# Kernel optimization log

Hardware: AMD Instinct MI355X
Metric: run time of the kernel (lower is better)

Reference implementation:

```python
import jax, jax.numpy as jnp
import numpy as np
from jax import lax

COST_CLASS, COST_BBOX, COST_GIOU = 1.0, 5.0, 2.0
BIG = 1e30  # stand-in for +inf when masking assigned rows/cols


def box_cxcywh_to_xyxy(b):
    cx, cy, w, h = b[..., 0], b[..., 1], b[..., 2], b[..., 3]
    return jnp.stack([cx - 0.5 * w, cy - 0.5 * h, cx + 0.5 * w, cy + 0.5 * h], axis=-1)


def generalized_box_iou(boxes1, boxes2):
    # boxes1: [Q,4] xyxy, boxes2: [T,4] xyxy -> [Q,T]
    area1 = jnp.clip(boxes1[:, 2] - boxes1[:, 0], 0) * jnp.clip(boxes1[:, 3] - boxes1[:, 1], 0)
    area2 = jnp.clip(boxes2[:, 2] - boxes2[:, 0], 0) * jnp.clip(boxes2[:, 3] - boxes2[:, 1], 0)
    lt = jnp.maximum(boxes1[:, None, :2], boxes2[None, :, :2])
    rb = jnp.minimum(boxes1[:, None, 2:], boxes2[None, :, 2:])
    wh = jnp.clip(rb - lt, 0)
    inter = wh[..., 0] * wh[..., 1]
    union = area1[:, None] + area2[None, :] - inter
    iou = inter / jnp.clip(union, 1e-6)
    lt_e = jnp.minimum(boxes1[:, None, :2], boxes2[None, :, :2])
    rb_e = jnp.maximum(boxes1[:, None, 2:], boxes2[None, :, 2:])
    wh_e = jnp.clip(rb_e - lt_e, 0)
    area = wh_e[..., 0] * wh_e[..., 1]
    return iou - (area - union) / jnp.clip(area, 1e-6)


def build_cost(pred_logits, pred_boxes, tgt_labels, tgt_boxes):
    # pred_logits [B,Q,C], pred_boxes [B,Q,4] cxcywh, tgt_labels [B,T], tgt_boxes [B,T,4]
    B, Q, C = pred_logits.shape
    T = tgt_labels.shape[1]
    out_prob = jax.nn.softmax(pred_logits, axis=-1)                       # [B,Q,C]
    idx = jnp.broadcast_to(tgt_labels[:, None, :], (B, Q, T))
    cost_class = -jnp.take_along_axis(out_prob, idx, axis=2)              # [B,Q,T]
    cost_bbox = jnp.sum(jnp.abs(pred_boxes[:, :, None, :] - tgt_boxes[:, None, :, :]), axis=-1)
    giou = jax.vmap(generalized_box_iou)(box_cxcywh_to_xyxy(pred_boxes), box_cxcywh_to_xyxy(tgt_boxes))
    return COST_CLASS * cost_class + COST_BBOX * cost_bbox + COST_GIOU * (-giou)


def greedy_assignment(cost):
    # cost [Q,T] -> (src_idx [n], tgt_idx [n]) with n = min(Q,T); GPU-resident scan
    Q, T = cost.shape
    n = min(Q, T)

    def step(c, _):
        flat = jnp.argmin(c)
        i = flat // T
        j = flat % T
        c = c.at[i, :].set(BIG).at[:, j].set(BIG)
        return c, (i.astype(jnp.int64), j.astype(jnp.int64))

    _, (src, tgt) = lax.scan(step, cost, None, length=n)
    return src, tgt


def setup_inputs() -> dict:
    key = jax.random.key(0)
    k1, k2, k3, k4 = jax.random.split(key, 4)
    B, Q, C, T = 64, 900, 256, 100
    pred_logits = jax.random.normal(k1, (B, Q, C), dtype=jnp.float32)
    pred_boxes = jax.random.uniform(k2, (B, Q, 4), dtype=jnp.float32)   # cxcywh in [0,1)
    tgt_labels = jax.random.randint(k3, (B, T), 0, C)
    tgt_boxes = jax.random.uniform(k4, (B, T, 4), dtype=jnp.float32)
    return {"pred_logits": pred_logits, "pred_boxes": pred_boxes,
            "tgt_labels": tgt_labels, "tgt_boxes": tgt_boxes}


def reference(pred_logits, pred_boxes, tgt_labels, tgt_boxes):
    cost = build_cost(pred_logits, pred_boxes, tgt_labels, tgt_boxes)   # [B,Q,T]
    src_idx, tgt_idx = jax.vmap(greedy_assignment)(cost)                # [B,n] each
    return cost, src_idx, tgt_idx
```

## Files before the change

kernel.cpp:

```cpp
#include <hip/hip_runtime.h>
#include <math.h>

#define B_ 64
#define Q_ 900
#define C_ 256
#define T_ 100
#define N_ 100
#define BIGF 1.0e30f
#define ROWS_PER_LANE 15
#define CHUNKS 15

typedef unsigned int u32;
typedef unsigned long long ull;

__device__ inline u32 hm_ordf(float v) {
    u32 u = __float_as_uint(v);
    return (u & 0x80000000u) ? ~u : (u | 0x80000000u);
}
__device__ inline ull hm_ikey(float v, int r, int t) {
    return ~(((ull)hm_ordf(v) << 18) | ((ull)(u32)r << 7) | (ull)(u32)t);
}

__global__ __launch_bounds__(256) void hm_cost_colmin(
    const float* __restrict__ logits,
    const float* __restrict__ pboxes,
    const int*   __restrict__ tlabels,
    const float* __restrict__ tboxes,
    float* __restrict__ cost,
    ull* __restrict__ part)
{
    int bc   = blockIdx.x;
    int b    = bc / CHUNKS;
    int c    = bc % CHUNKS;
    int lane = threadIdx.x & 63;
    int wid  = threadIdx.x >> 6;
    int r0   = c * 64;
    int R    = Q_ - r0; if (R > 64) R = 64;

    __shared__ double s_exp[4][C_];
    __shared__ ull    s_part[4][128][2];

    int ta = lane, tb = 64 + lane;
    bool hb = (tb < T_);
    int laba = tlabels[b * T_ + ta];
    int labb = hb ? tlabels[b * T_ + tb] : 0;
    const float* tba = tboxes + ((size_t)b * T_ + ta) * 4;
    const float* tbb = tboxes + ((size_t)b * T_ + (hb ? tb : 0)) * 4;
    double tcxa = tba[0], tcya = tba[1], twa = tba[2], tha = tba[3];
    double tcxb = tbb[0], tcyb = tbb[1], twb = tbb[2], thb_ = tbb[3];
    double txa1 = tcxa - 0.5 * twa, tya1 = tcya - 0.5 * tha;
    double txa2 = tcxa + 0.5 * twa, tya2 = tcya + 0.5 * tha;
    double txb1 = tcxb - 0.5 * twb, tyb1 = tcyb - 0.5 * thb_;
    double txb2 = tcxb + 0.5 * twb, tyb2 = tcyb + 0.5 * thb_;
    double area2a = fmax(txa2 - txa1, 0.0) * fmax(tya2 - tya1, 0.0);
    double area2b = fmax(txb2 - txb1, 0.0) * fmax(tyb2 - tyb1, 0.0);

    ull ka1 = 0ull, ka2 = 0ull;
    ull kb1 = 0ull, kb2 = 0ull;

    for (int r = r0 + wid; r < r0 + R; r += 4) {
        int bq = b * Q_ + r;

        const float* row = logits + (size_t)bq * C_;
        float v[4];
        float m = -INFINITY;
#pragma unroll
        for (int i = 0; i < 4; ++i) {
            v[i] = row[lane + 64 * i];
            m = fmaxf(m, v[i]);
        }
#pragma unroll
        for (int off = 32; off >= 1; off >>= 1)
            m = fmaxf(m, __shfl_xor(m, off, 64));

        double e[4];
        double s = 0.0;
#pragma unroll
        for (int i = 0; i < 4; ++i) {
            e[i] = exp((double)v[i] - (double)m);
            s += e[i];
        }
#pragma unroll
        for (int off = 32; off >= 1; off >>= 1)
            s += __shfl_xor(s, off, 64);

#pragma unroll
        for (int i = 0; i < 4; ++i)
            s_exp[wid][lane + 64 * i] = e[i];

        const float* pb = pboxes + (size_t)bq * 4;
        double pcx = pb[0], pcy = pb[1], pw = pb[2], ph = pb[3];
        double px1 = pcx - 0.5 * pw, py1 = pcy - 0.5 * ph;
        double px2 = pcx + 0.5 * pw, py2 = pcy + 0.5 * ph;
        double area1 = fmax(px2 - px1, 0.0) * fmax(py2 - py1, 0.0);

        {
            double prob = s_exp[wid][laba] / s;
            double l1 = fabs(pcx - tcxa) + fabs(pcy - tcya) + fabs(pw - twa) + fabs(ph - tha);
            double iw = fmax(fmin(px2, txa2) - fmax(px1, txa1), 0.0);
            double ih = fmax(fmin(py2, tya2) - fmax(py1, tya1), 0.0);
            double inter = iw * ih;
            double uni = area1 + area2a - inter;
            double iou = inter / fmax(uni, 1e-6);
            double ew = fmax(fmax(px2, txa2) - fmin(px1, txa1), 0.0);
            double eh = fmax(fmax(py2, tya2) - fmin(py1, tya1), 0.0);
            double earea = ew * eh;
            double giou = iou - (earea - uni) / fmax(earea, 1e-6);
            double cst = -prob + 5.0 * l1 - 2.0 * giou;
            float cf = (float)cst;
            cost[(size_t)bq * T_ + ta] = cf;
            ull kk = hm_ikey(cf, r, ta);
            if (kk > ka1) { ka2 = ka1; ka1 = kk; }
            else if (kk > ka2) ka2 = kk;
        }
        if (hb) {
            double prob = s_exp[wid][labb] / s;
            double l1 = fabs(pcx - tcxb) + fabs(pcy - tcyb) + fabs(pw - twb) + fabs(ph - thb_);
            double iw = fmax(fmin(px2, txb2) - fmax(px1, txb1), 0.0);
            double ih = fmax(fmin(py2, tyb2) - fmax(py1, tyb1), 0.0);
            double inter = iw * ih;
            double uni = area1 + area2b - inter;
            double iou = inter / fmax(uni, 1e-6);
            double ew = fmax(fmax(px2, txb2) - fmin(px1, txb1), 0.0);
            double eh = fmax(fmax(py2, tyb2) - fmin(py1, tyb1), 0.0);
            double earea = ew * eh;
            double giou = iou - (earea - uni) / fmax(earea, 1e-6);
            double cst = -prob + 5.0 * l1 - 2.0 * giou;
            float cf = (float)cst;
            cost[(size_t)bq * T_ + tb] = cf;
            ull kk = hm_ikey(cf, r, tb);
            if (kk > kb1) { kb2 = kb1; kb1 = kk; }
            else if (kk > kb2) kb2 = kk;
        }
    }

    s_part[wid][lane][0]      = ka1;
    s_part[wid][lane][1]      = ka2;
    s_part[wid][64 + lane][0] = kb1;
    s_part[wid][64 + lane][1] = kb2;
    __syncthreads();
    int tid = threadIdx.x;
    if (tid < T_) {
        ull b1 = 0ull, b2 = 0ull;
#pragma unroll
        for (int w = 0; w < 4; ++w) {
#pragma unroll
            for (int j = 0; j < 2; ++j) {
                ull cc = s_part[w][tid][j];
                if (cc > b1) { b2 = b1; b1 = cc; }
                else if (cc > b2) b2 = cc;
            }
        }
        ull* dst = part + (((size_t)b * CHUNKS + c) * T_ + tid) * 2;
        dst[0] = b1;
        dst[1] = b2;
    }
}

template <int CTRL>
__device__ inline ull hm_dpp64(ull x) {
    u32 lo = (u32)x, hi = (u32)(x >> 32);
    lo = (u32)__builtin_amdgcn_update_dpp(0, (int)lo, CTRL, 0xF, 0xF, false);
    hi = (u32)__builtin_amdgcn_update_dpp(0, (int)hi, CTRL, 0xF, 0xF, false);
    return ((ull)hi << 32) | lo;
}

__device__ inline ull hm_wave_max_chain(ull x) {
    ull p;
    p = hm_dpp64<0x111>(x); x = (p > x) ? p : x;
    p = hm_dpp64<0x112>(x); x = (p > x) ? p : x;
    p = hm_dpp64<0x114>(x); x = (p > x) ? p : x;
    p = hm_dpp64<0x118>(x); x = (p > x) ? p : x;
    p = hm_dpp64<0x142>(x); x = (p > x) ? p : x;
    p = hm_dpp64<0x143>(x); x = (p > x) ? p : x;
    return x;
}

__device__ inline u32 hm_wave_max_lo(ull x) {
    x = hm_wave_max_chain(x);
    return (u32)__builtin_amdgcn_readlane((int)(u32)x, 63);
}
__device__ inline ull hm_wave_max_full(ull x) {
    x = hm_wave_max_chain(x);
    u32 lo = (u32)__builtin_amdgcn_readlane((int)(u32)x, 63);
    u32 hi = (u32)__builtin_amdgcn_readlane((int)(u32)(x >> 32), 63);
    return ((ull)hi << 32) | lo;
}

__global__ __launch_bounds__(64) void hm_greedy_top2k(
    const float* __restrict__ cost,
    const ull* __restrict__ part,
    float* __restrict__ out_src,
    float* __restrict__ out_tgt)
{
    int b = blockIdx.x;
    int l = threadIdx.x;
    const float* Cb = cost + (size_t)b * Q_ * T_;

    int  t0 = l, t1 = 64 + l;
    bool a1 = (t1 < T_);

    ull c1a = 0ull, c2a = 0ull, c1b = 0ull, c2b = 0ull;
#pragma unroll
    for (int c = 0; c < CHUNKS; ++c) {
        const ull* p0 = part + (((size_t)b * CHUNKS + c) * T_ + t0) * 2;
#pragma unroll
        for (int j = 0; j < 2; ++j) {
            ull cc = p0[j];
            if (cc > c1a) { c2a = c1a; c1a = cc; }
            else if (cc > c2a) c2a = cc;
        }
        if (a1) {
            const ull* p1 = part + (((size_t)b * CHUNKS + c) * T_ + t1) * 2;
#pragma unroll
            for (int j = 0; j < 2; ++j) {
                ull cc = p1[j];
                if (cc > c1b) { c2b = c1b; c1b = cc; }
                else if (cc > c2b) c2b = cc;
            }
        }
    }

    unsigned removed = 0u;
    float* os = out_src + b * N_;
    float* ot = out_tgt + b * N_;

    int k = 0;
    while (k < N_) {
        ull cmax = (c1a > c1b) ? c1a : c1b;
        u32 winlo = hm_wave_max_lo(cmax);
        u32 keylo = ~winlo;
        int t = (int)(keylo & 127u);
        int q = (int)((keylo >> 7) & 1023u);

        if ((keylo >> 17) & 1u) {
            ull b1 = 0ull, b2 = 0ull;
#pragma unroll
            for (int i = 0; i < ROWS_PER_LANE; ++i) {
                int r = l + 64 * i;
                bool ok = (r < Q_) && !((removed >> i) & 1u);
                float v = ok ? Cb[(size_t)r * T_ + t] : BIGF;
                ull ik = ok ? hm_ikey(v, r, t) : 0ull;
                if (ik > b1) { b2 = b1; b1 = ik; }
                else if (ik > b2) b2 = ik;
            }
            ull w1 = hm_wave_max_full(b1);
            ull alt = (b1 == w1) ? b2 : b1;
            ull w2 = hm_wave_max_full(alt);
            if (t0 == t) { c1a = w1; c2a = w2; }
            if (t1 == t) { c1b = w1; c2b = w2; }
            continue;
        }

        if (l == 0) { os[k] = (float)q; ot[k] = (float)t; }
        if ((q & 63) == l) removed |= 1u << (q >> 6);

        {
            u32 r1 = ((~(u32)c1a) >> 7) & 1023u;
            u32 r2 = ((~(u32)c2a) >> 7) & 1023u;
            bool die1 = (r1 == (u32)q);
            bool die2 = (r2 == (u32)q);
            ull st2 = c2a & ~(1ull << 17);
            ull nc1 = die1 ? c2a : c1a;
            ull nc2 = (die1 || die2) ? st2 : c2a;
            bool kill = (t0 == t);
            c1a = kill ? 0ull : nc1;
            c2a = kill ? 0ull : nc2;
        }
        {
            u32 r1 = ((~(u32)c1b) >> 7) & 1023u;
            u32 r2 = ((~(u32)c2b) >> 7) & 1023u;
            bool die1 = (r1 == (u32)q);
            bool die2 = (r2 == (u32)q);
            ull st2 = c2b & ~(1ull << 17);
            ull nc1 = die1 ? c2b : c1b;
            ull nc2 = (die1 || die2) ? st2 : c2b;
            bool kill = (t1 == t);
            c1b = kill ? 0ull : nc1;
            c2b = kill ? 0ull : nc2;
        }

        ++k;
    }
}

extern "C" void kernel_launch(void* const* d_in, const int* in_sizes, int n_in,
                              void* d_out, int out_size, void* d_ws, size_t ws_size,
                              hipStream_t stream)
{
    const float* pred_logits = (const float*)d_in[0];
    const float* pred_boxes  = (const float*)d_in[1];
    const int*   tgt_labels  = (const int*)d_in[2];
    const float* tgt_boxes   = (const float*)d_in[3];

    float* out_cost = (float*)d_out;
    float* out_src  = out_cost + (size_t)B_ * Q_ * T_;
    float* out_tgt  = out_src  + (size_t)B_ * N_;

    ull* part = (ull*)d_ws;

    hm_cost_colmin<<<B_ * CHUNKS, 256, 0, stream>>>(pred_logits, pred_boxes,
                                                    tgt_labels, tgt_boxes,
                                                    out_cost, part);

    hm_greedy_top2k<<<B_, 64, 0, stream>>>(out_cost, part, out_src, out_tgt);
}
```

Measured before the change: 104.7 us.

## Use fp32 cost math, finer row chunks, and two-batch interleaved greedy wave

The cost kernel switches from double to float arithmetic and splits each batch into 25 chunks of 36 rows instead of 15 chunks of 64. The greedy kernel now handles two batches per wave, interleaving their DPP reductions to hide latency. It also splits each 64-bit key into a 32-bit value reduction followed by an id reduction, and buffers outputs in registers until the end. Float math may change tie-breaking and assignments compared with the double-precision path, and half as many greedy blocks run.

```diff
diff --git a/kernel.cpp b/kernel.cpp
--- a/kernel.cpp
+++ b/kernel.cpp
@@ -8,7 +8,8 @@
 #define N_ 100
 #define BIGF 1.0e30f
 #define ROWS_PER_LANE 15
-#define CHUNKS 15
+#define CHUNKS 25
+#define RPC 36
 
 typedef unsigned int u32;
 typedef unsigned long long ull;
@@ -21,7 +22,7 @@
     return ~(((ull)hm_ordf(v) << 18) | ((ull)(u32)r << 7) | (ull)(u32)t);
 }
 
-__global__ __launch_bounds__(256) void hm_cost_colmin(
+__global__ __launch_bounds__(256) void hm_cost_colmin_f32(
     const float* __restrict__ logits,
     const float* __restrict__ pboxes,
     const int*   __restrict__ tlabels,
@@ -34,11 +35,10 @@
     int c    = bc % CHUNKS;
     int lane = threadIdx.x & 63;
     int wid  = threadIdx.x >> 6;
-    int r0   = c * 64;
-    int R    = Q_ - r0; if (R > 64) R = 64;
-
-    __shared__ double s_exp[4][C_];
-    __shared__ ull    s_part[4][128][2];
+    int r0   = c * RPC;
+
+    __shared__ float s_exp[4][C_];
+    __shared__ ull   s_part[4][128][2];
 
     int ta = lane, tb = 64 + lane;
     bool hb = (tb < T_);
@@ -46,19 +46,19 @@
     int labb = hb ? tlabels[b * T_ + tb] : 0;
     const float* tba = tboxes + ((size_t)b * T_ + ta) * 4;
     const float* tbb = tboxes + ((size_t)b * T_ + (hb ? tb : 0)) * 4;
-    double tcxa = tba[0], tcya = tba[1], twa = tba[2], tha = tba[3];
-    double tcxb = tbb[0], tcyb = tbb[1], twb = tbb[2], thb_ = tbb[3];
-    double txa1 = tcxa - 0.5 * twa, tya1 = tcya - 0.5 * tha;
-    double txa2 = tcxa + 0.5 * twa, tya2 = tcya + 0.5 * tha;
-    double txb1 = tcxb - 0.5 * twb, tyb1 = tcyb - 0.5 * thb_;
-    double txb2 = tcxb + 0.5 * twb, tyb2 = tcyb + 0.5 * thb_;
-    double area2a = fmax(txa2 - txa1, 0.0) * fmax(tya2 - tya1, 0.0);
-    double area2b = fmax(txb2 - txb1, 0.0) * fmax(tyb2 - tyb1, 0.0);
+    float tcxa = tba[0], tcya = tba[1], twa = tba[2], tha = tba[3];
+    float tcxb = tbb[0], tcyb = tbb[1], twb = tbb[2], thb_ = tbb[3];
+    float txa1 = tcxa - 0.5f * twa, tya1 = tcya - 0.5f * tha;
+    float txa2 = tcxa + 0.5f * twa, tya2 = tcya + 0.5f * tha;
+    float txb1 = tcxb - 0.5f * twb, tyb1 = tcyb - 0.5f * thb_;
+    float txb2 = tcxb + 0.5f * twb, tyb2 = tcyb + 0.5f * thb_;
+    float area2a = fmaxf(txa2 - txa1, 0.0f) * fmaxf(tya2 - tya1, 0.0f);
+    float area2b = fmaxf(txb2 - txb1, 0.0f) * fmaxf(tyb2 - tyb1, 0.0f);
 
     ull ka1 = 0ull, ka2 = 0ull;
     ull kb1 = 0ull, kb2 = 0ull;
 
-    for (int r = r0 + wid; r < r0 + R; r += 4) {
+    for (int r = r0 + wid; r < r0 + RPC; r += 4) {
         int bq = b * Q_ + r;
 
         const float* row = logits + (size_t)bq * C_;
@@ -73,11 +73,11 @@
         for (int off = 32; off >= 1; off >>= 1)
             m = fmaxf(m, __shfl_xor(m, off, 64));
 
-        double e[4];
-        double s = 0.0;
+        float e[4];
+        float s = 0.0f;
 #pragma unroll
         for (int i = 0; i < 4; ++i) {
-            e[i] = exp((double)v[i] - (double)m);
+            e[i] = expf(v[i] - m);
             s += e[i];
         }
 #pragma unroll
@@ -89,44 +89,42 @@
             s_exp[wid][lane + 64 * i] = e[i];
 
         const float* pb = pboxes + (size_t)bq * 4;
-        double pcx = pb[0], pcy = pb[1], pw = pb[2], ph = pb[3];
-        double px1 = pcx - 0.5 * pw, py1 = pcy - 0.5 * ph;
-        double px2 = pcx + 0.5 * pw, py2 = pcy + 0.5 * ph;
-        double area1 = fmax(px2 - px1, 0.0) * fmax(py2 - py1, 0.0);
+        float pcx = pb[0], pcy = pb[1], pw = pb[2], ph = pb[3];
+        float px1 = pcx - 0.5f * pw, py1 = pcy - 0.5f * ph;
+        float px2 = pcx + 0.5f * pw, py2 = pcy + 0.5f * ph;
+        float area1 = fmaxf(px2 - px1, 0.0f) * fmaxf(py2 - py1, 0.0f);
 
         {
-            double prob = s_exp[wid][laba] / s;
-            double l1 = fabs(pcx - tcxa) + fabs(pcy - tcya) + fabs(pw - twa) + fabs(ph - tha);
-            double iw = fmax(fmin(px2, txa2) - fmax(px1, txa1), 0.0);
-            double ih = fmax(fmin(py2, tya2) - fmax(py1, tya1), 0.0);
-            double inter = iw * ih;
-            double uni = area1 + area2a - inter;
-            double iou = inter / fmax(uni, 1e-6);
-            double ew = fmax(fmax(px2, txa2) - fmin(px1, txa1), 0.0);
-            double eh = fmax(fmax(py2, tya2) - fmin(py1, tya1), 0.0);
-            double earea = ew * eh;
-            double giou = iou - (earea - uni) / fmax(earea, 1e-6);
-            double cst = -prob + 5.0 * l1 - 2.0 * giou;
-            float cf = (float)cst;
+            float prob = s_exp[wid][laba] / s;
+            float l1 = fabsf(pcx - tcxa) + fabsf(pcy - tcya) + fabsf(pw - twa) + fabsf(ph - tha);
+            float iw = fmaxf(fminf(px2, txa2) - fmaxf(px1, txa1), 0.0f);
+            float ih = fmaxf(fminf(py2, tya2) - fmaxf(py1, tya1), 0.0f);
+            float inter = iw * ih;
+            float uni = area1 + area2a - inter;
+            float iou = inter / fmaxf(uni, 1e-6f);
+            float ew = fmaxf(fmaxf(px2, txa2) - fminf(px1, txa1), 0.0f);
+            float eh = fmaxf(fmaxf(py2, tya2) - fminf(py1, tya1), 0.0f);
+            float earea = ew * eh;
+            float giou = iou - (earea - uni) / fmaxf(earea, 1e-6f);
+            float cf = -prob + 5.0f * l1 - 2.0f * giou;
             cost[(size_t)bq * T_ + ta] = cf;
             ull kk = hm_ikey(cf, r, ta);
             if (kk > ka1) { ka2 = ka1; ka1 = kk; }
             else if (kk > ka2) ka2 = kk;
         }
         if (hb) {
-            double prob = s_exp[wid][labb] / s;
-            double l1 = fabs(pcx - tcxb) + fabs(pcy - tcyb) + fabs(pw - twb) + fabs(ph - thb_);
-            double iw = fmax(fmin(px2, txb2) - fmax(px1, txb1), 0.0);
-            double ih = fmax(fmin(py2, tyb2) - fmax(py1, tyb1), 0.0);
-            double inter = iw * ih;
-            double uni = area1 + area2b - inter;
-            double iou = inter / fmax(uni, 1e-6);
-            double ew = fmax(fmax(px2, txb2) - fmin(px1, txb1), 0.0);
-            double eh = fmax(fmax(py2, tyb2) - fmin(py1, tyb1), 0.0);
-            double earea = ew * eh;
-            double giou = iou - (earea - uni) / fmax(earea, 1e-6);
-            double cst = -prob + 5.0 * l1 - 2.0 * giou;
-            float cf = (float)cst;
+            float prob = s_exp[wid][labb] / s;
+            float l1 = fabsf(pcx - tcxb) + fabsf(pcy - tcyb) + fabsf(pw - twb) + fabsf(ph - thb_);
+            float iw = fmaxf(fminf(px2, txb2) - fmaxf(px1, txb1), 0.0f);
+            float ih = fmaxf(fminf(py2, tyb2) - fmaxf(py1, tyb1), 0.0f);
+            float inter = iw * ih;
+            float uni = area1 + area2b - inter;
+            float iou = inter / fmaxf(uni, 1e-6f);
+            float ew = fmaxf(fmaxf(px2, txb2) - fminf(px1, txb1), 0.0f);
+            float eh = fmaxf(fmaxf(py2, tyb2) - fminf(py1, tyb1), 0.0f);
+            float earea = ew * eh;
+            float giou = iou - (earea - uni) / fmaxf(earea, 1e-6f);
+            float cf = -prob + 5.0f * l1 - 2.0f * giou;
             cost[(size_t)bq * T_ + tb] = cf;
             ull kk = hm_ikey(cf, r, tb);
             if (kk > kb1) { kb2 = kb1; kb1 = kk; }
@@ -157,6 +155,14 @@
     }
 }
 
+__device__ inline u32 hm_umax32(u32 a, u32 b) { return a > b ? a : b; }
+
+template <int CTRL>
+__device__ inline u32 hm_stage(u32 x) {
+    u32 p = (u32)__builtin_amdgcn_update_dpp(0, (int)x, CTRL, 0xF, 0xF, false);
+    return x > p ? x : p;
+}
+
 template <int CTRL>
 __device__ inline ull hm_dpp64(ull x) {
     u32 lo = (u32)x, hi = (u32)(x >> 32);
@@ -164,8 +170,7 @@
     hi = (u32)__builtin_amdgcn_update_dpp(0, (int)hi, CTRL, 0xF, 0xF, false);
     return ((ull)hi << 32) | lo;
 }
-
-__device__ inline ull hm_wave_max_chain(ull x) {
+__device__ inline ull hm_wave_max_full64(ull x) {
     ull p;
     p = hm_dpp64<0x111>(x); x = (p > x) ? p : x;
     p = hm_dpp64<0x112>(x); x = (p > x) ? p : x;
@@ -173,114 +178,232 @@
     p = hm_dpp64<0x118>(x); x = (p > x) ? p : x;
     p = hm_dpp64<0x142>(x); x = (p > x) ? p : x;
     p = hm_dpp64<0x143>(x); x = (p > x) ? p : x;
-    return x;
-}
-
-__device__ inline u32 hm_wave_max_lo(ull x) {
-    x = hm_wave_max_chain(x);
-    return (u32)__builtin_amdgcn_readlane((int)(u32)x, 63);
-}
-__device__ inline ull hm_wave_max_full(ull x) {
-    x = hm_wave_max_chain(x);
     u32 lo = (u32)__builtin_amdgcn_readlane((int)(u32)x, 63);
     u32 hi = (u32)__builtin_amdgcn_readlane((int)(u32)(x >> 32), 63);
     return ((ull)hi << 32) | lo;
 }
 
-__global__ __launch_bounds__(64) void hm_greedy_top2k(
+__global__ __launch_bounds__(64) void hm_greedy_g2(
     const float* __restrict__ cost,
     const ull* __restrict__ part,
     float* __restrict__ out_src,
     float* __restrict__ out_tgt)
 {
-    int b = blockIdx.x;
+    int bp = blockIdx.x;
+    int b0 = bp * 2, b1 = bp * 2 + 1;
     int l = threadIdx.x;
-    const float* Cb = cost + (size_t)b * Q_ * T_;
+    const float* C0 = cost + (size_t)b0 * Q_ * T_;
+    const float* C1 = cost + (size_t)b1 * Q_ * T_;
 
     int  t0 = l, t1 = 64 + l;
     bool a1 = (t1 < T_);
 
-    ull c1a = 0ull, c2a = 0ull, c1b = 0ull, c2b = 0ull;
+    ull pA1_0 = 0ull, pA2_0 = 0ull, pB1_0 = 0ull, pB2_0 = 0ull;
+    ull pA1_1 = 0ull, pA2_1 = 0ull, pB1_1 = 0ull, pB2_1 = 0ull;
 #pragma unroll
     for (int c = 0; c < CHUNKS; ++c) {
-        const ull* p0 = part + (((size_t)b * CHUNKS + c) * T_ + t0) * 2;
+        const ull* q0 = part + (((size_t)b0 * CHUNKS + c) * T_ + t0) * 2;
+        const ull* q1 = part + (((size_t)b1 * CHUNKS + c) * T_ + t0) * 2;
 #pragma unroll
         for (int j = 0; j < 2; ++j) {
-            ull cc = p0[j];
-            if (cc > c1a) { c2a = c1a; c1a = cc; }
-            else if (cc > c2a) c2a = cc;
+            ull cc = q0[j];
+            if (cc > pA1_0) { pA2_0 = pA1_0; pA1_0 = cc; } else if (cc > pA2_0) pA2_0 = cc;
+            ull dd = q1[j];
+            if (dd > pA1_1) { pA2_1 = pA1_1; pA1_1 = dd; } else if (dd > pA2_1) pA2_1 = dd;
         }
         if (a1) {
-            const ull* p1 = part + (((size_t)b * CHUNKS + c) * T_ + t1) * 2;
+            const ull* r0p = part + (((size_t)b0 * CHUNKS + c) * T_ + t1) * 2;
+            const ull* r1p = part + (((size_t)b1 * CHUNKS + c) * T_ + t1) * 2;
 #pragma unroll
             for (int j = 0; j < 2; ++j) {
-                ull cc = p1[j];
-                if (cc > c1b) { c2b = c1b; c1b = cc; }
-                else if (cc > c2b) c2b = cc;
+                ull cc = r0p[j];
+                if (cc > pB1_0) { pB2_0 = pB1_0; pB1_0 = cc; } else if (cc > pB2_0) pB2_0 = cc;
+                ull dd = r1p[j];
+                if (dd > pB1_1) { pB2_1 = pB1_1; pB1_1 = dd; } else if (dd > pB2_1) pB2_1 = dd;
             }
         }
     }
 
-    unsigned removed = 0u;
-    float* os = out_src + b * N_;
-    float* ot = out_tgt + b * N_;
-
-    int k = 0;
-    while (k < N_) {
-        ull cmax = (c1a > c1b) ? c1a : c1b;
-        u32 winlo = hm_wave_max_lo(cmax);
-        u32 keylo = ~winlo;
-        int t = (int)(keylo & 127u);
-        int q = (int)((keylo >> 7) & 1023u);
-
-        if ((keylo >> 17) & 1u) {
-            ull b1 = 0ull, b2 = 0ull;
-#pragma unroll
-            for (int i = 0; i < ROWS_PER_LANE; ++i) {
-                int r = l + 64 * i;
-                bool ok = (r < Q_) && !((removed >> i) & 1u);
-                float v = ok ? Cb[(size_t)r * T_ + t] : BIGF;
-                ull ik = ok ? hm_ikey(v, r, t) : 0ull;
-                if (ik > b1) { b2 = b1; b1 = ik; }
-                else if (ik > b2) b2 = ik;
+    u32 ya0  = ~((u32)((~pA1_0) >> 18)), ida0  = (u32)(~pA1_0) & 0x3FFFFu;
+    u32 y2a0 = ~((u32)((~pA2_0) >> 18)), id2a0 = (u32)(~pA2_0) & 0x3FFFFu;
+    u32 yb0  = a1 ? ~((u32)((~pB1_0) >> 18)) : 0u;
+    u32 idb0 = a1 ? ((u32)(~pB1_0) & 0x3FFFFu) : 0x3FFFFu;
+    u32 y2b0 = a1 ? ~((u32)((~pB2_0) >> 18)) : 0u;
+    u32 id2b0 = a1 ? ((u32)(~pB2_0) & 0x3FFFFu) : 0x3FFFFu;
+    u32 ya1  = ~((u32)((~pA1_1) >> 18)), ida1  = (u32)(~pA1_1) & 0x3FFFFu;
+    u32 y2a1 = ~((u32)((~pA2_1) >> 18)), id2a1 = (u32)(~pA2_1) & 0x3FFFFu;
+    u32 yb1  = a1 ? ~((u32)((~pB1_1) >> 18)) : 0u;
+    u32 idb1 = a1 ? ((u32)(~pB1_1) & 0x3FFFFu) : 0x3FFFFu;
+    u32 y2b1 = a1 ? ~((u32)((~pB2_1) >> 18)) : 0u;
+    u32 id2b1 = a1 ? ((u32)(~pB2_1) & 0x3FFFFu) : 0x3FFFFu;
+
+    unsigned rem0 = 0u, rem1 = 0u;
+    u32 pk00 = 0u, pk01 = 0u, pk10 = 0u, pk11 = 0u;
+    int k0 = 0, k1 = 0;
+
+    while (k0 < N_ || k1 < N_) {
+        u32 x0 = (k0 < N_) ? hm_umax32(ya0, yb0) : 0u;
+        u32 x1 = (k1 < N_) ? hm_umax32(ya1, yb1) : 0u;
+        x0 = hm_stage<0x111>(x0); x1 = hm_stage<0x111>(x1);
+        x0 = hm_stage<0x112>(x0); x1 = hm_stage<0x112>(x1);
+        x0 = hm_stage<0x114>(x0); x1 = hm_stage<0x114>(x1);
+        x0 = hm_stage<0x118>(x0); x1 = hm_stage<0x118>(x1);
+        x0 = hm_stage<0x142>(x0); x1 = hm_stage<0x142>(x1);
+        x0 = hm_stage<0x143>(x0); x1 = hm_stage<0x143>(x1);
+        u32 winy0 = (u32)__builtin_amdgcn_readlane((int)x0, 63);
+        u32 winy1 = (u32)__builtin_amdgcn_readlane((int)x1, 63);
+
+        u32 za0 = (ya0 == winy0) ? ~ida0 : 0u;
+        u32 zb0 = (yb0 == winy0) ? ~idb0 : 0u;
+        u32 z0 = hm_umax32(za0, zb0);
+        u32 za1 = (ya1 == winy1) ? ~ida1 : 0u;
+        u32 zb1 = (yb1 == winy1) ? ~idb1 : 0u;
+        u32 z1 = hm_umax32(za1, zb1);
+        z0 = hm_stage<0x111>(z0); z1 = hm_stage<0x111>(z1);
+        z0 = hm_stage<0x112>(z0); z1 = hm_stage<0x112>(z1);
+        z0 = hm_stage<0x114>(z0); z1 = hm_stage<0x114>(z1);
+        z0 = hm_stage<0x118>(z0); z1 = hm_stage<0x118>(z1);
+        z0 = hm_stage<0x142>(z0); z1 = hm_stage<0x142>(z1);
+        z0 = hm_stage<0x143>(z0); z1 = hm_stage<0x143>(z1);
+        u32 winid0 = (~(u32)__builtin_amdgcn_readlane((int)z0, 63)) & 0x3FFFFu;
+        u32 winid1 = (~(u32)__builtin_amdgcn_readlane((int)z1, 63)) & 0x3FFFFu;
+
+        if (k0 < N_) {
+            int t = (int)(winid0 & 127u);
+            int q = (int)((winid0 >> 7) & 1023u);
+            if (winid0 & 0x20000u) {
+                ull b1k = 0ull, b2k = 0ull;
+#pragma unroll
+                for (int i = 0; i < ROWS_PER_LANE; ++i) {
+                    int r = l + 64 * i;
+                    bool ok = (r < Q_) && !((rem0 >> i) & 1u);
+                    float v = ok ? C0[(size_t)r * T_ + t] : BIGF;
+                    ull ik = ok ? hm_ikey(v, r, t) : 0ull;
+                    if (ik > b1k) { b2k = b1k; b1k = ik; }
+                    else if (ik > b2k) b2k = ik;
+                }
+                ull w1 = hm_wave_max_full64(b1k);
+                ull alt = (b1k == w1) ? b2k : b1k;
+                ull w2 = hm_wave_max_full64(alt);
+                if (t0 == t) {
+                    ya0  = ~((u32)((~w1) >> 18)); ida0  = (u32)(~w1) & 0x3FFFFu;
+                    y2a0 = ~((u32)((~w2) >> 18)); id2a0 = (u32)(~w2) & 0x3FFFFu;
+                }
+                if (t1 == t) {
+                    yb0  = ~((u32)((~w1) >> 18)); idb0  = (u32)(~w1) & 0x3FFFFu;
+                    y2b0 = ~((u32)((~w2) >> 18)); id2b0 = (u32)(~w2) & 0x3FFFFu;
+                }
+            } else {
+                u32 qt = winid0 & 0x1FFFFu;
+                if (k0 < 64) { if (l == k0)        pk00 = qt; }
+                else         { if (l == (k0 & 63)) pk01 = qt; }
+                if ((q & 63) == l) rem0 |= 1u << (q >> 6);
+                {
+                    bool die1 = (((ida0  >> 7) & 1023u) == (u32)q);
+                    bool die2 = (((id2a0 >> 7) & 1023u) == (u32)q);
+                    u32 nya  = die1 ? y2a0  : ya0;
+                    u32 nida = die1 ? id2a0 : ida0;
+                    u32 nid2 = (die1 || die2) ? (id2a0 | 0x20000u) : id2a0;
+                    bool kill = (t0 == t);
+                    ya0   = kill ? 0u       : nya;
+                    ida0  = kill ? 0x3FFFFu : nida;
+                    y2a0  = kill ? 0u       : y2a0;
+                    id2a0 = kill ? 0x3FFFFu : nid2;
+                }
+                {
+                    bool die1 = (((idb0  >> 7) & 1023u) == (u32)q);
+                    bool die2 = (((id2b0 >> 7) & 1023u) == (u32)q);
+                    u32 nyb  = die1 ? y2b0  : yb0;
+                    u32 nidb = die1 ? id2b0 : idb0;
+                    u32 nid2 = (die1 || die2) ? (id2b0 | 0x20000u) : id2b0;
+                    bool kill = (t1 == t);
+                    yb0   = kill ? 0u       : nyb;
+                    idb0  = kill ? 0x3FFFFu : nidb;
+                    y2b0  = kill ? 0u       : y2b0;
+                    id2b0 = kill ? 0x3FFFFu : nid2;
+                }
+                ++k0;
             }
-            ull w1 = hm_wave_max_full(b1);
-            ull alt = (b1 == w1) ? b2 : b1;
-            ull w2 = hm_wave_max_full(alt);
-            if (t0 == t) { c1a = w1; c2a = w2; }
-            if (t1 == t) { c1b = w1; c2b = w2; }
-            continue;
-        }
-
-        if (l == 0) { os[k] = (float)q; ot[k] = (float)t; }
-        if ((q & 63) == l) removed |= 1u << (q >> 6);
-
-        {
-            u32 r1 = ((~(u32)c1a) >> 7) & 1023u;
-            u32 r2 = ((~(u32)c2a) >> 7) & 1023u;
-            bool die1 = (r1 == (u32)q);
-            bool die2 = (r2 == (u32)q);
-            ull st2 = c2a & ~(1ull << 17);
-            ull nc1 = die1 ? c2a : c1a;
-            ull nc2 = (die1 || die2) ? st2 : c2a;
-            bool kill = (t0 == t);
-            c1a = kill ? 0ull : nc1;
-            c2a = kill ? 0ull : nc2;
-        }
-        {
-            u32 r1 = ((~(u32)c1b) >> 7) & 1023u;
-            u32 r2 = ((~(u32)c2b) >> 7) & 1023u;
-            bool die1 = (r1 == (u32)q);
-            bool die2 = (r2 == (u32)q);
-            ull st2 = c2b & ~(1ull << 17);
-            ull nc1 = die1 ? c2b : c1b;
-            ull nc2 = (die1 || die2) ? st2 : c2b;
-            bool kill = (t1 == t);
-            c1b = kill ? 0ull : nc1;
-            c2b = kill ? 0ull : nc2;
-        }
-
-        ++k;
+        }
+
+        if (k1 < N_) {
+            int t = (int)(winid1 & 127u);
+            int q = (int)((winid1 >> 7) & 1023u);
+            if (winid1 & 0x20000u) {
+                ull b1k = 0ull, b2k = 0ull;
+#pragma unroll
+                for (int i = 0; i < ROWS_PER_LANE; ++i) {
+                    int r = l + 64 * i;
+                    bool ok = (r < Q_) && !((rem1 >> i) & 1u);
+                    float v = ok ? C1[(size_t)r * T_ + t] : BIGF;
+                    ull ik = ok ? hm_ikey(v, r, t) : 0ull;
+                    if (ik > b1k) { b2k = b1k; b1k = ik; }
+                    else if (ik > b2k) b2k = ik;
+                }
+                ull w1 = hm_wave_max_full64(b1k);
+                ull alt = (b1k == w1) ? b2k : b1k;
+                ull w2 = hm_wave_max_full64(alt);
+                if (t0 == t) {
+                    ya1  = ~((u32)((~w1) >> 18)); ida1  = (u32)(~w1) & 0x3FFFFu;
+                    y2a1 = ~((u32)((~w2) >> 18)); id2a1 = (u32)(~w2) & 0x3FFFFu;
+                }
+                if (t1 == t) {
+                    yb1  = ~((u32)((~w1) >> 18)); idb1  = (u32)(~w1) & 0x3FFFFu;
+                    y2b1 = ~((u32)((~w2) >> 18)); id2b1 = (u32)(~w2) & 0x3FFFFu;
+                }
+            } else {
+                u32 qt = winid1 & 0x1FFFFu;
+                if (k1 < 64) { if (l == k1)        pk10 = qt; }
+                else         { if (l == (k1 & 63)) pk11 = qt; }
+                if ((q & 63) == l) rem1 |= 1u << (q >> 6);
+                {
+                    bool die1 = (((ida1  >> 7) & 1023u) == (u32)q);
+                    bool die2 = (((id2a1 >> 7) & 1023u) == (u32)q);
+                    u32 nya  = die1 ? y2a1  : ya1;
+                    u32 nida = die1 ? id2a1 : ida1;
+                    u32 nid2 = (die1 || die2) ? (id2a1 | 0x20000u) : id2a1;
+                    bool kill = (t0 == t);
+                    ya1   = kill ? 0u       : nya;
+                    ida1  = kill ? 0x3FFFFu : nida;
+                    y2a1  = kill ? 0u       : y2a1;
+                    id2a1 = kill ? 0x3FFFFu : nid2;
+                }
+                {
+                    bool die1 = (((idb1  >> 7) & 1023u) == (u32)q);
+                    bool die2 = (((id2b1 >> 7) & 1023u) == (u32)q);
+                    u32 nyb  = die1 ? y2b1  : yb1;
+                    u32 nidb = die1 ? id2b1 : idb1;
+                    u32 nid2 = (die1 || die2) ? (id2b1 | 0x20000u) : id2b1;
+                    bool kill = (t1 == t);
+                    yb1   = kill ? 0u       : nyb;
+                    idb1  = kill ? 0x3FFFFu : nidb;
+                    y2b1  = kill ? 0u       : y2b1;
+                    id2b1 = kill ? 0x3FFFFu : nid2;
+                }
+                ++k1;
+            }
+        }
+    }
+
+    {
+        float* os = out_src + b0 * N_;
+        float* ot = out_tgt + b0 * N_;
+        os[l] = (float)(pk00 >> 7);
+        ot[l] = (float)(pk00 & 127u);
+        if (l < N_ - 64) {
+            os[64 + l] = (float)(pk01 >> 7);
+            ot[64 + l] = (float)(pk01 & 127u);
+        }
+    }
+    {
+        float* os = out_src + b1 * N_;
+        float* ot = out_tgt + b1 * N_;
+        os[l] = (float)(pk10 >> 7);
+        ot[l] = (float)(pk10 & 127u);
+        if (l < N_ - 64) {
+            os[64 + l] = (float)(pk11 >> 7);
+            ot[64 + l] = (float)(pk11 & 127u);
+        }
     }
 }
 
@@ -299,9 +422,9 @@
 
     ull* part = (ull*)d_ws;
 
-    hm_cost_colmin<<<B_ * CHUNKS, 256, 0, stream>>>(pred_logits, pred_boxes,
-                                                    tgt_labels, tgt_boxes,
-                                                    out_cost, part);
-
-    hm_greedy_top2k<<<B_, 64, 0, stream>>>(out_cost, part, out_src, out_tgt);
-}
+    hm_cost_colmin_f32<<<B_ * CHUNKS, 256, 0, stream>>>(pred_logits, pred_boxes,
+                                                        tgt_labels, tgt_boxes,
+                                                        out_cost, part);
+
+    hm_greedy_g2<<<B_ / 2, 64, 0, stream>>>(out_cost, part, out_src, out_tgt);
+}
```

After: 118.3 us. +13.0%, slower.

## Switch cost kernel to fp32, rebalance chunks, and use sorted-head greedy assignment

Applied to the files above, without the earlier changes.

The cost kernel now computes softmax, L1 and GIoU in single precision instead of double, which removes slow FP64 math. Rows per block go from 64 to 36, giving 25 chunks per batch and more blocks. The greedy kernel is rewritten so that it rank-sorts per-column minima once and then walks the sorted head, keeping a small overflow set refreshed by the stored second-best entry or by a column rescan. This replaces the per-step wave-wide argmax. The risks are fp32 rounding changing the cost values or tie order, and extra complexity in the assignment logic.

```diff
diff --git a/kernel.cpp b/kernel.cpp
--- a/kernel.cpp
+++ b/kernel.cpp
@@ -8,7 +8,9 @@
 #define N_ 100
 #define BIGF 1.0e30f
 #define ROWS_PER_LANE 15
-#define CHUNKS 15
+#define CHUNKS 25
+#define RPC 36
+#define MAXK 0xFFFFFFFFFFFFFFFFull
 
 typedef unsigned int u32;
 typedef unsigned long long ull;
@@ -21,7 +23,7 @@
     return ~(((ull)hm_ordf(v) << 18) | ((ull)(u32)r << 7) | (ull)(u32)t);
 }
 
-__global__ __launch_bounds__(256) void hm_cost_colmin(
+__global__ __launch_bounds__(256) void hm_cost_colmin_f32(
     const float* __restrict__ logits,
     const float* __restrict__ pboxes,
     const int*   __restrict__ tlabels,
@@ -34,11 +36,10 @@
     int c    = bc % CHUNKS;
     int lane = threadIdx.x & 63;
     int wid  = threadIdx.x >> 6;
-    int r0   = c * 64;
-    int R    = Q_ - r0; if (R > 64) R = 64;
-
-    __shared__ double s_exp[4][C_];
-    __shared__ ull    s_part[4][128][2];
+    int r0   = c * RPC;
+
+    __shared__ float s_exp[4][C_];
+    __shared__ ull   s_part[4][128][2];
 
     int ta = lane, tb = 64 + lane;
     bool hb = (tb < T_);
@@ -46,19 +47,19 @@
     int labb = hb ? tlabels[b * T_ + tb] : 0;
     const float* tba = tboxes + ((size_t)b * T_ + ta) * 4;
     const float* tbb = tboxes + ((size_t)b * T_ + (hb ? tb : 0)) * 4;
-    double tcxa = tba[0], tcya = tba[1], twa = tba[2], tha = tba[3];
-    double tcxb = tbb[0], tcyb = tbb[1], twb = tbb[2], thb_ = tbb[3];
-    double txa1 = tcxa - 0.5 * twa, tya1 = tcya - 0.5 * tha;
-    double txa2 = tcxa + 0.5 * twa, tya2 = tcya + 0.5 * tha;
-    double txb1 = tcxb - 0.5 * twb, tyb1 = tcyb - 0.5 * thb_;
-    double txb2 = tcxb + 0.5 * twb, tyb2 = tcyb + 0.5 * thb_;
-    double area2a = fmax(txa2 - txa1, 0.0) * fmax(tya2 - tya1, 0.0);
-    double area2b = fmax(txb2 - txb1, 0.0) * fmax(tyb2 - tyb1, 0.0);
+    float tcxa = tba[0], tcya = tba[1], twa = tba[2], tha = tba[3];
+    float tcxb = tbb[0], tcyb = tbb[1], twb = tbb[2], thb_ = tbb[3];
+    float txa1 = tcxa - 0.5f * twa, tya1 = tcya - 0.5f * tha;
+    float txa2 = tcxa + 0.5f * twa, tya2 = tcya + 0.5f * tha;
+    float txb1 = tcxb - 0.5f * twb, tyb1 = tcyb - 0.5f * thb_;
+    float txb2 = tcxb + 0.5f * twb, tyb2 = tcyb + 0.5f * thb_;
+    float area2a = fmaxf(txa2 - txa1, 0.0f) * fmaxf(tya2 - tya1, 0.0f);
+    float area2b = fmaxf(txb2 - txb1, 0.0f) * fmaxf(tyb2 - tyb1, 0.0f);
 
     ull ka1 = 0ull, ka2 = 0ull;
     ull kb1 = 0ull, kb2 = 0ull;
 
-    for (int r = r0 + wid; r < r0 + R; r += 4) {
+    for (int r = r0 + wid; r < r0 + RPC; r += 4) {
         int bq = b * Q_ + r;
 
         const float* row = logits + (size_t)bq * C_;
@@ -73,11 +74,11 @@
         for (int off = 32; off >= 1; off >>= 1)
             m = fmaxf(m, __shfl_xor(m, off, 64));
 
-        double e[4];
-        double s = 0.0;
+        float e[4];
+        float s = 0.0f;
 #pragma unroll
         for (int i = 0; i < 4; ++i) {
-            e[i] = exp((double)v[i] - (double)m);
+            e[i] = expf(v[i] - m);
             s += e[i];
         }
 #pragma unroll
@@ -89,44 +90,42 @@
             s_exp[wid][lane + 64 * i] = e[i];
 
         const float* pb = pboxes + (size_t)bq * 4;
-        double pcx = pb[0], pcy = pb[1], pw = pb[2], ph = pb[3];
-        double px1 = pcx - 0.5 * pw, py1 = pcy - 0.5 * ph;
-        double px2 = pcx + 0.5 * pw, py2 = pcy + 0.5 * ph;
-        double area1 = fmax(px2 - px1, 0.0) * fmax(py2 - py1, 0.0);
+        float pcx = pb[0], pcy = pb[1], pw = pb[2], ph = pb[3];
+        float px1 = pcx - 0.5f * pw, py1 = pcy - 0.5f * ph;
+        float px2 = pcx + 0.5f * pw, py2 = pcy + 0.5f * ph;
+        float area1 = fmaxf(px2 - px1, 0.0f) * fmaxf(py2 - py1, 0.0f);
 
         {
-            double prob = s_exp[wid][laba] / s;
-            double l1 = fabs(pcx - tcxa) + fabs(pcy - tcya) + fabs(pw - twa) + fabs(ph - tha);
-            double iw = fmax(fmin(px2, txa2) - fmax(px1, txa1), 0.0);
-            double ih = fmax(fmin(py2, tya2) - fmax(py1, tya1), 0.0);
-            double inter = iw * ih;
-            double uni = area1 + area2a - inter;
-            double iou = inter / fmax(uni, 1e-6);
-            double ew = fmax(fmax(px2, txa2) - fmin(px1, txa1), 0.0);
-            double eh = fmax(fmax(py2, tya2) - fmin(py1, tya1), 0.0);
-            double earea = ew * eh;
-            double giou = iou - (earea - uni) / fmax(earea, 1e-6);
-            double cst = -prob + 5.0 * l1 - 2.0 * giou;
-            float cf = (float)cst;
+            float prob = s_exp[wid][laba] / s;
+            float l1 = fabsf(pcx - tcxa) + fabsf(pcy - tcya) + fabsf(pw - twa) + fabsf(ph - tha);
+            float iw = fmaxf(fminf(px2, txa2) - fmaxf(px1, txa1), 0.0f);
+            float ih = fmaxf(fminf(py2, tya2) - fmaxf(py1, tya1), 0.0f);
+            float inter = iw * ih;
+            float uni = area1 + area2a - inter;
+            float iou = inter / fmaxf(uni, 1e-6f);
+            float ew = fmaxf(fmaxf(px2, txa2) - fminf(px1, txa1), 0.0f);
+            float eh = fmaxf(fmaxf(py2, tya2) - fminf(py1, tya1), 0.0f);
+            float earea = ew * eh;
+            float giou = iou - (earea - uni) / fmaxf(earea, 1e-6f);
+            float cf = -prob + 5.0f * l1 - 2.0f * giou;
             cost[(size_t)bq * T_ + ta] = cf;
             ull kk = hm_ikey(cf, r, ta);
             if (kk > ka1) { ka2 = ka1; ka1 = kk; }
             else if (kk > ka2) ka2 = kk;
         }
         if (hb) {
-            double prob = s_exp[wid][labb] / s;
-            double l1 = fabs(pcx - tcxb) + fabs(pcy - tcyb) + fabs(pw - twb) + fabs(ph - thb_);
-            double iw = fmax(fmin(px2, txb2) - fmax(px1, txb1), 0.0);
-            double ih = fmax(fmin(py2, tyb2) - fmax(py1, tyb1), 0.0);
-            double inter = iw * ih;
-            double uni = area1 + area2b - inter;
-            double iou = inter / fmax(uni, 1e-6);
-            double ew = fmax(fmax(px2, txb2) - fmin(px1, txb1), 0.0);
-            double eh = fmax(fmax(py2, tyb2) - fmin(py1, tyb1), 0.0);
-            double earea = ew * eh;
-            double giou = iou - (earea - uni) / fmax(earea, 1e-6);
-            double cst = -prob + 5.0 * l1 - 2.0 * giou;
-            float cf = (float)cst;
+            float prob = s_exp[wid][labb] / s;
+            float l1 = fabsf(pcx - tcxb) + fabsf(pcy - tcyb) + fabsf(pw - twb) + fabsf(ph - thb_);
+            float iw = fmaxf(fminf(px2, txb2) - fmaxf(px1, txb1), 0.0f);
+            float ih = fmaxf(fminf(py2, tyb2) - fmaxf(py1, tyb1), 0.0f);
+            float inter = iw * ih;
+            float uni = area1 + area2b - inter;
+            float iou = inter / fmaxf(uni, 1e-6f);
+            float ew = fmaxf(fmaxf(px2, txb2) - fminf(px1, txb1), 0.0f);
+            float eh = fmaxf(fmaxf(py2, tyb2) - fminf(py1, tyb1), 0.0f);
+            float earea = ew * eh;
+            float giou = iou - (earea - uni) / fmaxf(earea, 1e-6f);
+            float cf = -prob + 5.0f * l1 - 2.0f * giou;
             cost[(size_t)bq * T_ + tb] = cf;
             ull kk = hm_ikey(cf, r, tb);
             if (kk > kb1) { kb2 = kb1; kb1 = kk; }
@@ -164,8 +163,7 @@
     hi = (u32)__builtin_amdgcn_update_dpp(0, (int)hi, CTRL, 0xF, 0xF, false);
     return ((ull)hi << 32) | lo;
 }
-
-__device__ inline ull hm_wave_max_chain(ull x) {
+__device__ inline ull hm_wave_max_full64(ull x) {
     ull p;
     p = hm_dpp64<0x111>(x); x = (p > x) ? p : x;
     p = hm_dpp64<0x112>(x); x = (p > x) ? p : x;
@@ -173,21 +171,38 @@
     p = hm_dpp64<0x118>(x); x = (p > x) ? p : x;
     p = hm_dpp64<0x142>(x); x = (p > x) ? p : x;
     p = hm_dpp64<0x143>(x); x = (p > x) ? p : x;
-    return x;
-}
-
-__device__ inline u32 hm_wave_max_lo(ull x) {
-    x = hm_wave_max_chain(x);
-    return (u32)__builtin_amdgcn_readlane((int)(u32)x, 63);
-}
-__device__ inline ull hm_wave_max_full(ull x) {
-    x = hm_wave_max_chain(x);
     u32 lo = (u32)__builtin_amdgcn_readlane((int)(u32)x, 63);
     u32 hi = (u32)__builtin_amdgcn_readlane((int)(u32)(x >> 32), 63);
     return ((ull)hi << 32) | lo;
 }
 
-__global__ __launch_bounds__(64) void hm_greedy_top2k(
+__device__ inline ull hm_ov_min(ull a, ull b) {
+    ull x = ~a, y = ~b;
+    ull z = (x > y) ? x : y;
+    return ~hm_wave_max_full64(z);
+}
+
+__device__ inline ull hm_rescan(const float* Cb, int t, u32 removed, int l) {
+    ull best = 0ull;
+#pragma unroll
+    for (int i = 0; i < ROWS_PER_LANE; ++i) {
+        int r = l + 64 * i;
+        bool ok = (r < Q_) && !((removed >> i) & 1u);
+        float v = ok ? Cb[(size_t)r * T_ + t] : BIGF;
+        ull ik = ok ? hm_ikey(v, r, t) : 0ull;
+        best = (ik > best) ? ik : best;
+    }
+    return ~hm_wave_max_full64(best);
+}
+
+__device__ inline void hm_ov_insert(ull ins, int l, ull& ovK0, ull& ovK1) {
+    int t2 = (int)((u32)ins & 127u);
+    int owner = t2 & 63;
+    if (t2 < 64) { if (l == owner) ovK0 = ins; }
+    else         { if (l == owner) ovK1 = ins; }
+}
+
+__global__ __launch_bounds__(64) void hm_greedy_sorted(
     const float* __restrict__ cost,
     const ull* __restrict__ part,
     float* __restrict__ out_src,
@@ -200,87 +215,177 @@
     int  t0 = l, t1 = 64 + l;
     bool a1 = (t1 < T_);
 
-    ull c1a = 0ull, c2a = 0ull, c1b = 0ull, c2b = 0ull;
+    __shared__ ull s_key[128];
+    __shared__ ull s_pay[128];
+
+    ull i1a = 0ull, i2a = 0ull, i1b = 0ull, i2b = 0ull;
 #pragma unroll
     for (int c = 0; c < CHUNKS; ++c) {
         const ull* p0 = part + (((size_t)b * CHUNKS + c) * T_ + t0) * 2;
 #pragma unroll
         for (int j = 0; j < 2; ++j) {
             ull cc = p0[j];
-            if (cc > c1a) { c2a = c1a; c1a = cc; }
-            else if (cc > c2a) c2a = cc;
+            if (cc > i1a) { i2a = i1a; i1a = cc; }
+            else if (cc > i2a) i2a = cc;
         }
         if (a1) {
             const ull* p1 = part + (((size_t)b * CHUNKS + c) * T_ + t1) * 2;
 #pragma unroll
             for (int j = 0; j < 2; ++j) {
                 ull cc = p1[j];
-                if (cc > c1b) { c2b = c1b; c1b = cc; }
-                else if (cc > c2b) c2b = cc;
+                if (cc > i1b) { i2b = i1b; i1b = cc; }
+                else if (cc > i2b) i2b = cc;
             }
         }
     }
-
-    unsigned removed = 0u;
+    ull keyA = ~i1a, payA = ~i2a;
+    ull keyB = a1 ? ~i1b : (0xFFFFFFFFFFFFFF00ull | (ull)(u32)(64 + l));
+    ull payB = a1 ? ~i2b : MAXK;
+
+    s_key[l] = keyA;      s_pay[l] = payA;
+    s_key[64 + l] = keyB; s_pay[64 + l] = payB;
+    __syncthreads();
+
+    int rank0 = 0, rank1 = 0;
+#pragma unroll 4
+    for (int j = 0; j < 128; ++j) {
+        ull kj = s_key[j];
+        rank0 += (kj < keyA) ? 1 : 0;
+        rank1 += (kj < keyB) ? 1 : 0;
+    }
+    __syncthreads();
+    s_key[rank0] = keyA; s_pay[rank0] = payA;
+    s_key[rank1] = keyB; s_pay[rank1] = payB;
+    __syncthreads();
+
+    ull sk0 = s_key[l],      sp0 = s_pay[l];
+    ull sk1 = s_key[64 + l], sp1 = s_pay[64 + l];
+    int row0 = (int)(((u32)sk0 >> 7) & 1023u);
+    int row1 = (int)(((u32)sk1 >> 7) & 1023u);
+    bool v0 = true;
+    bool v1 = (l < T_ - 64);
+
+    ull validLo = ~0ull;
+    ull validHi = (1ull << (T_ - 64)) - 1ull;
+    ull ovK0 = MAXK, ovK1 = MAXK;
+    ull ovMin = MAXK;
+    u32 removed = 0u;
+    u32 pk0 = 0u, pk1 = 0u;
+
+    for (int k = 0; k < N_; ++k) {
+        int hr = -1;
+        if (validLo)      hr = __ffsll(validLo) - 1;
+        else if (validHi) hr = 64 + (__ffsll(validHi) - 1);
+        ull headKey = MAXK;
+        if (hr >= 0) {
+            int hl = hr & 63;
+            u32 klo, khi;
+            if (hr < 64) {
+                klo = (u32)__builtin_amdgcn_readlane((int)(u32)sk0, hl);
+                khi = (u32)__builtin_amdgcn_readlane((int)(u32)(sk0 >> 32), hl);
+            } else {
+                klo = (u32)__builtin_amdgcn_readlane((int)(u32)sk1, hl);
+                khi = (u32)__builtin_amdgcn_readlane((int)(u32)(sk1 >> 32), hl);
+            }
+            headKey = ((ull)khi << 32) | klo;
+        }
+
+        bool fromOv = (ovMin < headKey);
+        ull wkey = fromOv ? ovMin : headKey;
+        u32 wlo = (u32)wkey;
+        int t = (int)(wlo & 127u);
+        int q = (int)((wlo >> 7) & 1023u);
+
+        if (fromOv) {
+            int owner = t & 63;
+            if (t < 64) { if (l == owner) ovK0 = MAXK; }
+            else        { if (l == owner) ovK1 = MAXK; }
+            ovMin = hm_ov_min(ovK0, ovK1);
+        } else {
+            if (hr < 64) validLo &= ~(1ull << hr);
+            else         validHi &= ~(1ull << (hr - 64));
+            int hl = hr & 63;
+            if (l == hl) { if (hr < 64) v0 = false; else v1 = false; }
+        }
+
+        u32 qt = wlo & 0x1FFFFu;
+        if (k < 64) { if (l == k)        pk0 = qt; }
+        else        { if (l == (k & 63)) pk1 = qt; }
+        if ((q & 63) == l) removed |= 1u << (q >> 6);
+
+        bool hit = (v0 && row0 == q) || (v1 && row1 == q);
+        hit = hit || ((ovK0 != MAXK) && ((int)(((u32)ovK0 >> 7) & 1023u) == q));
+        hit = hit || ((ovK1 != MAXK) && ((int)(((u32)ovK1 >> 7) & 1023u) == q));
+        ull bal = __ballot(hit);
+
+        if (bal) {
+            ull mb = bal;
+            while (mb) {
+                int p = __ffsll(mb) - 1; mb &= mb - 1;
+                {
+                    int vv = (int)__builtin_amdgcn_readlane(v0 ? 1 : 0, p);
+                    int rr = (int)__builtin_amdgcn_readlane(row0, p);
+                    if (vv && rr == q) {
+                        validLo &= ~(1ull << p);
+                        if (l == p) v0 = false;
+                        u32 plo = (u32)__builtin_amdgcn_readlane((int)(u32)sp0, p);
+                        u32 phi = (u32)__builtin_amdgcn_readlane((int)(u32)(sp0 >> 32), p);
+                        ull pay = ((ull)phi << 32) | plo;
+                        int r2 = (int)(((u32)pay >> 7) & 1023u);
+                        u32 rm = (u32)__builtin_amdgcn_readlane((int)removed, r2 & 63);
+                        ull ins = (!((rm >> (r2 >> 6)) & 1u))
+                                  ? pay
+                                  : hm_rescan(Cb, (int)((u32)pay & 127u), removed, l);
+                        hm_ov_insert(ins, l, ovK0, ovK1);
+                    }
+                }
+                {
+                    int vv = (int)__builtin_amdgcn_readlane(v1 ? 1 : 0, p);
+                    int rr = (int)__builtin_amdgcn_readlane(row1, p);
+                    if (vv && rr == q) {
+                        validHi &= ~(1ull << p);
+                        if (l == p) v1 = false;
+                        u32 plo = (u32)__builtin_amdgcn_readlane((int)(u32)sp1, p);
+                        u32 phi = (u32)__builtin_amdgcn_readlane((int)(u32)(sp1 >> 32), p);
+                        ull pay = ((ull)phi << 32) | plo;
+                        int r2 = (int)(((u32)pay >> 7) & 1023u);
+                        u32 rm = (u32)__builtin_amdgcn_readlane((int)removed, r2 & 63);
+                        ull ins = (!((rm >> (r2 >> 6)) & 1u))
+                                  ? pay
+                                  : hm_rescan(Cb, (int)((u32)pay & 127u), removed, l);
+                        hm_ov_insert(ins, l, ovK0, ovK1);
+                    }
+                }
+                {
+                    u32 klo = (u32)__builtin_amdgcn_readlane((int)(u32)ovK0, p);
+                    u32 khi = (u32)__builtin_amdgcn_readlane((int)(u32)(ovK0 >> 32), p);
+                    ull ok = ((ull)khi << 32) | klo;
+                    if (ok != MAXK && ((int)(((u32)ok >> 7) & 1023u) == q)) {
+                        ull ins = hm_rescan(Cb, (int)((u32)ok & 127u), removed, l);
+                        hm_ov_insert(ins, l, ovK0, ovK1);
+                    }
+                }
+                {
+                    u32 klo = (u32)__builtin_amdgcn_readlane((int)(u32)ovK1, p);
+                    u32 khi = (u32)__builtin_amdgcn_readlane((int)(u32)(ovK1 >> 32), p);
+                    ull ok = ((ull)khi << 32) | klo;
+                    if (ok != MAXK && ((int)(((u32)ok >> 7) & 1023u) == q)) {
+                        ull ins = hm_rescan(Cb, (int)((u32)ok & 127u), removed, l);
+                        hm_ov_insert(ins, l, ovK0, ovK1);
+                    }
+                }
+            }
+            ovMin = hm_ov_min(ovK0, ovK1);
+        }
+    }
+
     float* os = out_src + b * N_;
     float* ot = out_tgt + b * N_;
-
-    int k = 0;
-    while (k < N_) {
-        ull cmax = (c1a > c1b) ? c1a : c1b;
-        u32 winlo = hm_wave_max_lo(cmax);
-        u32 keylo = ~winlo;
-        int t = (int)(keylo & 127u);
-        int q = (int)((keylo >> 7) & 1023u);
-
-        if ((keylo >> 17) & 1u) {
-            ull b1 = 0ull, b2 = 0ull;
-#pragma unroll
-            for (int i = 0; i < ROWS_PER_LANE; ++i) {
-                int r = l + 64 * i;
-                bool ok = (r < Q_) && !((removed >> i) & 1u);
-                float v = ok ? Cb[(size_t)r * T_ + t] : BIGF;
-                ull ik = ok ? hm_ikey(v, r, t) : 0ull;
-                if (ik > b1) { b2 = b1; b1 = ik; }
-                else if (ik > b2) b2 = ik;
-            }
-            ull w1 = hm_wave_max_full(b1);
-            ull alt = (b1 == w1) ? b2 : b1;
-            ull w2 = hm_wave_max_full(alt);
-            if (t0 == t) { c1a = w1; c2a = w2; }
-            if (t1 == t) { c1b = w1; c2b = w2; }
-            continue;
-        }
-
-        if (l == 0) { os[k] = (float)q; ot[k] = (float)t; }
-        if ((q & 63) == l) removed |= 1u << (q >> 6);
-
-        {
-            u32 r1 = ((~(u32)c1a) >> 7) & 1023u;
-            u32 r2 = ((~(u32)c2a) >> 7) & 1023u;
-            bool die1 = (r1 == (u32)q);
-            bool die2 = (r2 == (u32)q);
-            ull st2 = c2a & ~(1ull << 17);
-            ull nc1 = die1 ? c2a : c1a;
-            ull nc2 = (die1 || die2) ? st2 : c2a;
-            bool kill = (t0 == t);
-            c1a = kill ? 0ull : nc1;
-            c2a = kill ? 0ull : nc2;
-        }
-        {
-            u32 r1 = ((~(u32)c1b) >> 7) & 1023u;
-            u32 r2 = ((~(u32)c2b) >> 7) & 1023u;
-            bool die1 = (r1 == (u32)q);
-            bool die2 = (r2 == (u32)q);
-            ull st2 = c2b & ~(1ull << 17);
-            ull nc1 = die1 ? c2b : c1b;
-            ull nc2 = (die1 || die2) ? st2 : c2b;
-            bool kill = (t1 == t);
-            c1b = kill ? 0ull : nc1;
-            c2b = kill ? 0ull : nc2;
-        }
-
-        ++k;
+    os[l] = (float)(pk0 >> 7);
+    ot[l] = (float)(pk0 & 127u);
+    if (l < N_ - 64) {
+        os[64 + l] = (float)(pk1 >> 7);
+        ot[64 + l] = (float)(pk1 & 127u);
     }
 }
 
@@ -299,9 +404,9 @@
 
     ull* part = (ull*)d_ws;
 
-    hm_cost_colmin<<<B_ * CHUNKS, 256, 0, stream>>>(pred_logits, pred_boxes,
-                                                    tgt_labels, tgt_boxes,
-                                                    out_cost, part);
-
-    hm_greedy_top2k<<<B_, 64, 0, stream>>>(out_cost, part, out_src, out_tgt);
-}
+    hm_cost_colmin_f32<<<B_ * CHUNKS, 256, 0, stream>>>(pred_logits, pred_boxes,
+                                                        tgt_labels, tgt_boxes,
+                                                        out_cost, part);
+
+    hm_greedy_sorted<<<B_, 64, 0, stream>>>(out_cost, part, out_src, out_tgt);
+}
```

After: 104.6 us. Within noise of the previous version (-0.1%).
